# Optimization experiments

Hardware: AMD Instinct MI355X
Metric: run time of the kernel (lower is better)

The kernel has to match this reference:

```python
import jax, jax.numpy as jnp
import numpy as np

N = 50000      # nodes
DEG = 16       # avg degree
E = N * DEG    # edges
F_IN = 256
F_OUT = 128
ALPHA = 0.2    # leaky-relu slope


def setup_inputs() -> dict:
    key = jax.random.key(0)
    k1, k2, k3, k4, k5, k6 = jax.random.split(key, 6)
    x = jax.random.normal(k1, (N, F_IN), dtype=jnp.float32)
    # edges sorted by source (required by the module's `m` construction)
    src = jnp.repeat(jnp.arange(N, dtype=jnp.int32), DEG)
    dst = jax.random.randint(k2, (E,), 0, N, dtype=jnp.int32)
    edge = jnp.stack([src, dst])  # (2, E)
    s_w = 1.414 * np.sqrt(2.0 / (F_IN + F_OUT))   # xavier_normal gain=1.414
    s_a = 1.414 * np.sqrt(2.0 / (1 + 2 * F_OUT))
    W_high = jax.random.normal(k3, (F_IN, F_OUT), jnp.float32) * s_w
    W_low = jax.random.normal(k4, (F_IN, F_OUT), jnp.float32) * s_w
    a_high = jax.random.normal(k5, (1, 2 * F_OUT), jnp.float32) * s_a
    a_low = jax.random.normal(k6, (1, 2 * F_OUT), jnp.float32) * s_a
    return {"x": x, "edge": edge, "W_high": W_high, "W_low": W_low,
            "a_high": a_high, "a_low": a_low}


def _leaky(v):
    return jnp.where(v >= 0, v, ALPHA * v)


def _elu6(v):
    return jnp.minimum(jnp.where(v > 0, v, jnp.expm1(v)), 6.0)


def reference(x, edge, W_high, W_low, a_high, a_low):
    src, dst = edge[0], edge[1]
    n = x.shape[0]
    h_hi = x @ W_high            # (N, F_OUT)
    h_lo = x @ W_low

    # per-edge attention logits: a . [h[src], h[dst]]
    a_hi_s, a_hi_d = a_high[0, :F_OUT], a_high[0, F_OUT:]
    a_lo_s, a_lo_d = a_low[0, :F_OUT], a_low[0, F_OUT:]
    logit_hi = (h_hi @ a_hi_s)[src] + (h_hi @ a_hi_d)[dst]   # (E,)
    logit_lo = (h_lo @ a_lo_s)[src] + (h_lo @ a_lo_d)[dst]
    e_hi = jnp.exp(-_leaky(logit_hi))
    e_lo = jnp.exp(-_leaky(logit_lo))

    # sparse rowsum: spmm(edge, e, [N,N], ones) == segment_sum over src
    rowsum_hi = jax.ops.segment_sum(e_hi, src, num_segments=n)[:, None]
    rowsum_lo = jax.ops.segment_sum(e_lo, src, num_segments=n)[:, None]

    # relu6 (dropout p=0 / eval mode -> identity)
    e_hi = jnp.clip(e_hi, 0.0, 6.0)
    e_lo = jnp.clip(e_lo, 0.0, 6.0)

    # per-edge features, then m @ (.) == segment-sum of edge features by source
    he_hi = h_hi[src] + h_hi[dst]                # (E, F_OUT)
    he_lo = h_lo[src] - h_lo[dst]
    hn_hi = jax.ops.segment_sum(he_hi, src, num_segments=n)  # (N, F_OUT)
    hn_lo = jax.ops.segment_sum(he_lo, src, num_segments=n)

    # spmm(edge, e, [N,N], hn): row i sums e_ij * hn[j] over its edges
    hp_hi = jax.ops.segment_sum(e_hi[:, None] * hn_hi[dst], src, num_segments=n)
    hp_lo = jax.ops.segment_sum(e_lo[:, None] * hn_lo[dst], src, num_segments=n)

    hp_hi = hp_hi / (rowsum_hi + 1e-16)
    hp_lo = hp_lo / (rowsum_lo + 1e-16)
    h_prime = 0.5 * (hp_hi + hp_lo)
    return _elu6(h_prime)  # concat=True branch
```

## Files before the change

kernel.cpp:

```cpp
#include <hip/hip_runtime.h>
#include <hip/hip_bf16.h>
#include <math.h>

#define NN    50000
#define DEG   16
#define FIN   256
#define FOUT  128
#define EE    (NN * DEG)
#define ALPHA 0.2f

#define BM 64
#define BN 256

#define SLW 32

typedef __hip_bfloat16 bf16;
typedef _Float16 f16;
typedef __attribute__((ext_vector_type(8))) _Float16 f16x8;
typedef __attribute__((ext_vector_type(8))) short short8;
typedef __attribute__((ext_vector_type(4))) float f32x4;
typedef __attribute__((ext_vector_type(8))) unsigned short u16x8;
typedef __attribute__((ext_vector_type(8))) unsigned int u32x8;

__global__ __launch_bounds__(256) void split_w_kernel(
    const float* __restrict__ Wh, const float* __restrict__ Wl,
    bf16* __restrict__ Wcat2)
{
    const int k = blockIdx.x;
    const int n = threadIdx.x;
    const float w = (n < FOUT) ? Wh[(size_t)k * FOUT + n]
                               : Wl[(size_t)k * FOUT + (n - FOUT)];
    const bf16 hi = __float2bfloat16(w);
    const bf16 lo = __float2bfloat16(w - __bfloat162float(hi));
    Wcat2[(size_t)n * 512 + k]       = hi;
    Wcat2[(size_t)n * 512 + 256 + k] = lo;
}

__global__ __launch_bounds__(256) void gemm_mfma_kernel(
    const float* __restrict__ x, const bf16* __restrict__ Wcat2,
    const float* __restrict__ a_high, const float* __restrict__ a_low,
    f16* __restrict__ h16, float* __restrict__ sd_s, float* __restrict__ sd_d)
{
    __shared__ bf16 Ah[2][BM * 32];
    __shared__ bf16 Al[2][BM * 32];
    __shared__ bf16 Ba[2][BN * 32];
    __shared__ bf16 Bb[2][BN * 32];

    const int t    = threadIdx.x;
    const int lane = t & 63;
    const int w    = t >> 6;
    const int r0   = blockIdx.x * BM;

    f32x4 acc[4][4] = {};

    const int arow = t >> 2;
    const float* xsrc = x + (size_t)min(r0 + arow, NN - 1) * FIN + (t & 3) * 8;
    const int awaddr = arow * 64 + ((((t & 3)) + (arow >> 1)) & 3) * 16;

    int bro[4], bsl[4];
#pragma unroll
    for (int i = 0; i < 4; ++i) {
        const int idx = t + i * 256;
        bro[i] = idx >> 2;
        bsl[i] = ((idx & 3) - (bro[i] >> 1)) & 3;
    }

    const int lr = lane & 15, lg = lane >> 4;

    float4 xa = *(const float4*)(xsrc + 0);
    float4 xb = *(const float4*)(xsrc + 4);
#pragma unroll
    for (int i = 0; i < 4; ++i) {
        __builtin_amdgcn_global_load_lds(
            (const __attribute__((address_space(1))) void*)
                (Wcat2 + (size_t)bro[i] * 512 + 0 + bsl[i] * 8),
            (__attribute__((address_space(3))) void*)((char*)Ba[0] + (t + i * 256) * 16),
            16, 0, 0);
        __builtin_amdgcn_global_load_lds(
            (const __attribute__((address_space(1))) void*)
                (Wcat2 + (size_t)bro[i] * 512 + 256 + 0 + bsl[i] * 8),
            (__attribute__((address_space(3))) void*)((char*)Bb[0] + (t + i * 256) * 16),
            16, 0, 0);
    }
    {
        short8 hi8, lo8;
        const float f[8] = {xa.x, xa.y, xa.z, xa.w, xb.x, xb.y, xb.z, xb.w};
#pragma unroll
        for (int j = 0; j < 8; ++j) {
            const bf16 h = __float2bfloat16(f[j]);
            const bf16 l = __float2bfloat16(f[j] - __bfloat162float(h));
            ((bf16*)&hi8)[j] = h;
            ((bf16*)&lo8)[j] = l;
        }
        *(short8*)((char*)Ah[0] + awaddr) = hi8;
        *(short8*)((char*)Al[0] + awaddr) = lo8;
    }
    xa = *(const float4*)(xsrc + 32 + 0);
    xb = *(const float4*)(xsrc + 32 + 4);
    __syncthreads();

#pragma unroll
    for (int s = 0; s < 8; ++s) {
        const int cur = s & 1, nxt = cur ^ 1;

        if (s < 7) {
            short8 hi8, lo8;
            const float f[8] = {xa.x, xa.y, xa.z, xa.w, xb.x, xb.y, xb.z, xb.w};
#pragma unroll
            for (int j = 0; j < 8; ++j) {
                const bf16 h = __float2bfloat16(f[j]);
                const bf16 l = __float2bfloat16(f[j] - __bfloat162float(h));
                ((bf16*)&hi8)[j] = h;
                ((bf16*)&lo8)[j] = l;
            }
            *(short8*)((char*)Ah[nxt] + awaddr) = hi8;
            *(short8*)((char*)Al[nxt] + awaddr) = lo8;

            const int c1 = (s + 1) * 32;
#pragma unroll
            for (int i = 0; i < 4; ++i) {
                __builtin_amdgcn_global_load_lds(
                    (const __attribute__((address_space(1))) void*)
                        (Wcat2 + (size_t)bro[i] * 512 + c1 + bsl[i] * 8),
                    (__attribute__((address_space(3))) void*)((char*)Ba[nxt] + (t + i * 256) * 16),
                    16, 0, 0);
                __builtin_amdgcn_global_load_lds(
                    (const __attribute__((address_space(1))) void*)
                        (Wcat2 + (size_t)bro[i] * 512 + 256 + c1 + bsl[i] * 8),
                    (__attribute__((address_space(3))) void*)((char*)Bb[nxt] + (t + i * 256) * 16),
                    16, 0, 0);
            }
            if (s < 6) {
                xa = *(const float4*)(xsrc + (s + 2) * 32 + 0);
                xb = *(const float4*)(xsrc + (s + 2) * 32 + 4);
            }
        }

        short8 fh[4], wa[4], wb[4], fl[4];
#pragma unroll
        for (int mi = 0; mi < 4; ++mi) {
            const int row  = mi * 16 + lr;
            const int slot = (lg + (row >> 1)) & 3;
            fh[mi] = *(const short8*)((const char*)Ah[cur] + row * 64 + slot * 16);
        }
#pragma unroll
        for (int ni = 0; ni < 4; ++ni) {
            const int row  = w * 64 + ni * 16 + lr;
            const int slot = (lg + (row >> 1)) & 3;
            wa[ni] = *(const short8*)((const char*)Ba[cur] + row * 64 + slot * 16);
        }
#pragma unroll
        for (int mi = 0; mi < 4; ++mi)
#pragma unroll
            for (int ni = 0; ni < 4; ++ni)
                acc[mi][ni] = __builtin_amdgcn_mfma_f32_16x16x32_bf16(
                    fh[mi], wa[ni], acc[mi][ni], 0, 0, 0);
#pragma unroll
        for (int ni = 0; ni < 4; ++ni) {
            const int row  = w * 64 + ni * 16 + lr;
            const int slot = (lg + (row >> 1)) & 3;
            wb[ni] = *(const short8*)((const char*)Bb[cur] + row * 64 + slot * 16);
        }
#pragma unroll
        for (int mi = 0; mi < 4; ++mi)
#pragma unroll
            for (int ni = 0; ni < 4; ++ni)
                acc[mi][ni] = __builtin_amdgcn_mfma_f32_16x16x32_bf16(
                    fh[mi], wb[ni], acc[mi][ni], 0, 0, 0);
#pragma unroll
        for (int mi = 0; mi < 4; ++mi) {
            const int row  = mi * 16 + lr;
            const int slot = (lg + (row >> 1)) & 3;
            fl[mi] = *(const short8*)((const char*)Al[cur] + row * 64 + slot * 16);
        }
#pragma unroll
        for (int mi = 0; mi < 4; ++mi)
#pragma unroll
            for (int ni = 0; ni < 4; ++ni)
                acc[mi][ni] = __builtin_amdgcn_mfma_f32_16x16x32_bf16(
                    fl[mi], wa[ni], acc[mi][ni], 0, 0, 0);

        __syncthreads();
    }

    const int slc_base = (w < 2) ? w * 4 : (w - 2) * 4;
    const int off      = ((w < 2) ? 0 : 16) + lr;
#pragma unroll
    for (int mi = 0; mi < 4; ++mi) {
        const int rowb = r0 + mi * 16 + lg * 4;
#pragma unroll
        for (int r = 0; r < 4; ++r) {
            const int row = rowb + r;
            if (row >= NN) continue;
#pragma unroll
            for (int ni = 0; ni < 4; ++ni)
                h16[((size_t)(slc_base + ni) * NN + row) * SLW + off] =
                    (f16)acc[mi][ni][r];
        }
    }

    __syncthreads();

    const float* aa = (w < 2) ? a_high : a_low;
    const int cb = (w < 2) ? w * 64 : (w - 2) * 64;
    float as_[4], ad_[4];
#pragma unroll
    for (int ni = 0; ni < 4; ++ni) {
        as_[ni] = aa[cb + ni * 16 + lr];
        ad_[ni] = aa[FOUT + cb + ni * 16 + lr];
    }
    float* sred = (float*)Ah[0];
#pragma unroll
    for (int mi = 0; mi < 4; ++mi)
#pragma unroll
        for (int r = 0; r < 4; ++r) {
            float ps = 0.f, pd = 0.f;
#pragma unroll
            for (int ni = 0; ni < 4; ++ni) {
                ps += acc[mi][ni][r] * as_[ni];
                pd += acc[mi][ni][r] * ad_[ni];
            }
#pragma unroll
            for (int o = 1; o < 16; o <<= 1) {
                ps += __shfl_xor(ps, o);
                pd += __shfl_xor(pd, o);
            }
            if (lr == 0) {
                const int row = mi * 16 + lg * 4 + r;
                sred[(w * 2 + 0) * 64 + row] = ps;
                sred[(w * 2 + 1) * 64 + row] = pd;
            }
        }
    __syncthreads();
    if (t < 64) {
        const int row = r0 + t;
        if (row < NN) {
            const float s_hi = sred[0 * 64 + t] + sred[2 * 64 + t];
            const float d_hi = sred[1 * 64 + t] + sred[3 * 64 + t];
            const float s_lo = sred[4 * 64 + t] + sred[6 * 64 + t];
            const float d_lo = sred[5 * 64 + t] + sred[7 * 64 + t];
            ((float2*)sd_s)[row] = make_float2(s_hi, s_lo);
            ((float2*)sd_d)[row] = make_float2(d_hi, d_lo);
        }
    }
}

__global__ __launch_bounds__(256) void weight_kernel(
    const int* __restrict__ dst, const float* __restrict__ sd_s,
    const float* __restrict__ sd_d, unsigned short* __restrict__ d16,
    unsigned int* __restrict__ w32)
{
    const int wid  = (blockIdx.x * 256 + threadIdx.x) >> 6;
    const int lane = threadIdx.x & 63;
    if (wid >= NN) return;

    const int e    = lane & 15;
    const int d_my = dst[wid * DEG + e];
    const bool whi = (lane & 16) == 0;
    const float2 s2 = ((const float2*)sd_s)[wid];
    const float2 dd = ((const float2*)sd_d)[d_my];
    const float l   = whi ? (s2.x + dd.x) : (s2.y + dd.y);
    const float ev  = __expf(-(l >= 0.f ? l : ALPHA * l));

    float rs = ev;
    rs += __shfl_xor(rs, 1);
    rs += __shfl_xor(rs, 2);
    rs += __shfl_xor(rs, 4);
    rs += __shfl_xor(rs, 8);
    const float wn = fminf(ev, 6.f) / (rs + 1e-16f);
    const float wl = __shfl(wn, e + 16);

    if (lane < 16) {
        const f16 wh16 = (f16)wn, wl16 = (f16)wl;
        const unsigned a = *(const unsigned short*)&wh16;
        const unsigned b = *(const unsigned short*)&wl16;
        d16[wid * DEG + e] = (unsigned short)d_my;
        w32[wid * DEG + e] = a | (b << 16);
    }
}

__global__ __launch_bounds__(320) void hn_slice_kernel(
    const f16* __restrict__ h16, const unsigned short* __restrict__ d16,
    f16* __restrict__ hn16)
{
    const int sl    = blockIdx.x & 7;
    const int chunk = blockIdx.x >> 3;
    const int wv    = threadIdx.x >> 6;
    const int lane  = threadIdx.x & 63;
    const int k     = lane >> 3;
    const int c     = (lane >> 1) & 3;
    const int hf    = lane & 1;
    const int n     = (chunk * 5 + wv) * 8 + k;

    const char* hsl = (const char*)(h16 + (size_t)sl * NN * SLW);
    const float sgn = (c < 2) ? 1.f : -1.f;
    const unsigned coff = (unsigned)c * 16u;
    const unsigned noff = (unsigned)n * 64u + coff;

    const u16x8 d8 = *(const u16x8*)(d16 + n * DEG + hf * 8);
    const f16x8 own = *(const f16x8*)(hsl + noff);

    float acc[8] = {};
#pragma unroll
    for (int t = 0; t < 8; ++t) {
        const unsigned d = (unsigned)d8[t];
        const f16x8 g = *(const f16x8*)(hsl + (d * 64u + coff));
#pragma unroll
        for (int j = 0; j < 8; ++j) acc[j] = fmaf(sgn, (float)g[j], acc[j]);
    }
#pragma unroll
    for (int j = 0; j < 8; ++j) acc[j] += __shfl_xor(acc[j], 1);

    if (hf == 0) {
        f16x8 o;
#pragma unroll
        for (int j = 0; j < 8; ++j) o[j] = (f16)fmaf((float)own[j], 16.f, acc[j]);
        *(f16x8*)((char*)(hn16 + (size_t)sl * NN * SLW) + noff) = o;
    }
}

__global__ __launch_bounds__(320) void out_slice_kernel(
    const f16* __restrict__ hn16, const unsigned short* __restrict__ d16,
    const unsigned int* __restrict__ w32, float* __restrict__ out)
{
    const int sl    = blockIdx.x & 7;
    const int chunk = blockIdx.x >> 3;
    const int wv    = threadIdx.x >> 6;
    const int lane  = threadIdx.x & 63;
    const int k     = lane >> 3;
    const int c     = (lane >> 1) & 3;
    const int hf    = lane & 1;
    const int n     = (chunk * 5 + wv) * 8 + k;
    const bool chi  = (c < 2);

    const char* hsl = (const char*)(hn16 + (size_t)sl * NN * SLW);
    const unsigned coff = (unsigned)c * 16u;

    const u16x8 d8 = *(const u16x8*)(d16 + n * DEG + hf * 8);
    const u32x8 w8 = *(const u32x8*)(w32 + n * DEG + hf * 8);

    float acc[8] = {};
#pragma unroll
    for (int t = 0; t < 8; ++t) {
        const unsigned wp = w8[t];
        const unsigned short wu = chi ? (unsigned short)(wp & 0xffffu)
                                      : (unsigned short)(wp >> 16);
        const float w = (float)(*(const f16*)&wu);
        const f16x8 g = *(const f16x8*)(hsl + ((unsigned)d8[t] * 64u + coff));
#pragma unroll
        for (int j = 0; j < 8; ++j) acc[j] = fmaf(w, (float)g[j], acc[j]);
    }
#pragma unroll
    for (int j = 0; j < 8; ++j) acc[j] += __shfl_xor(acc[j], 1);

    float4 v0, v1;
#pragma unroll
    for (int j = 0; j < 8; ++j) {
        const float p = __shfl_xor(acc[j], 4);
        float v = 0.5f * (acc[j] + p);
        v = (v > 0.f) ? v : (__expf(v) - 1.f);
        v = fminf(v, 6.f);
        if (j < 4) ((float*)&v0)[j] = v; else ((float*)&v1)[j - 4] = v;
    }
    if (chi && hf == 0) {
        float* op = out + (size_t)n * FOUT + sl * 16 + c * 8;
        *(float4*)op       = v0;
        *(float4*)(op + 4) = v1;
    }
}

extern "C" void kernel_launch(void* const* d_in, const int* in_sizes, int n_in,
                              void* d_out, int out_size, void* d_ws, size_t ws_size,
                              hipStream_t stream)
{
    const float* x      = (const float*)d_in[0];
    const int*   edge   = (const int*)d_in[1];
    const float* Wh     = (const float*)d_in[2];
    const float* Wl     = (const float*)d_in[3];
    const float* a_high = (const float*)d_in[4];
    const float* a_low  = (const float*)d_in[5];
    const int*   dstv   = edge + EE;

    char* ws = (char*)d_ws;
    f16*   h16   = (f16*)ws;
    f16*   hn16  = (f16*)(ws + 25600000);
    bf16*  Wcat2 = (bf16*)(ws + 51200000);
    float* sd_s  = (float*)(ws + 51800000);
    float* sd_d  = (float*)(ws + 52200000);
    unsigned short* d16 = (unsigned short*)(ws + 52600000);
    unsigned int*   w32 = (unsigned int*)(ws + 54400000);

    split_w_kernel<<<dim3(256), dim3(256), 0, stream>>>(Wh, Wl, Wcat2);
    gemm_mfma_kernel<<<dim3((NN + BM - 1) / BM), dim3(256), 0, stream>>>(
        x, Wcat2, a_high, a_low, h16, sd_s, sd_d);
    weight_kernel<<<dim3((NN + 3) / 4), dim3(256), 0, stream>>>(dstv, sd_s, sd_d, d16, w32);
    hn_slice_kernel<<<dim3(8 * 1250), dim3(320), 0, stream>>>(h16, d16, hn16);
    out_slice_kernel<<<dim3(8 * 1250), dim3(320), 0, stream>>>(hn16, d16, w32, (float*)d_out);
}
```

Baseline: 130.3 us.

## Load GEMM weight fragments directly from global memory instead of staging in LDS

The GEMM kernel no longer stages the split hi/lo weight tiles through double-buffered shared memory with async global-to-LDS loads. Each wave now reads its own B fragments straight from global memory, which the weight matrix's small size should keep in L2. All eight x chunks are also loaded and split into bf16 hi/lo parts up front and held in registers. This cuts LDS footprint and the LDS traffic for B, which may raise occupancy, but it raises register pressure and exposes global-load latency on the MFMA path.

```diff
diff --git a/kernel.cpp b/kernel.cpp
--- a/kernel.cpp
+++ b/kernel.cpp
@@ -43,8 +43,6 @@
 {
     __shared__ bf16 Ah[2][BM * 32];
     __shared__ bf16 Al[2][BM * 32];
-    __shared__ bf16 Ba[2][BN * 32];
-    __shared__ bf16 Bb[2][BN * 32];
 
     const int t    = threadIdx.x;
     const int lane = t & 63;
@@ -57,46 +55,27 @@
     const float* xsrc = x + (size_t)min(r0 + arow, NN - 1) * FIN + (t & 3) * 8;
     const int awaddr = arow * 64 + ((((t & 3)) + (arow >> 1)) & 3) * 16;
 
-    int bro[4], bsl[4];
-#pragma unroll
-    for (int i = 0; i < 4; ++i) {
-        const int idx = t + i * 256;
-        bro[i] = idx >> 2;
-        bsl[i] = ((idx & 3) - (bro[i] >> 1)) & 3;
-    }
-
     const int lr = lane & 15, lg = lane >> 4;
 
-    float4 xa = *(const float4*)(xsrc + 0);
-    float4 xb = *(const float4*)(xsrc + 4);
-#pragma unroll
-    for (int i = 0; i < 4; ++i) {
-        __builtin_amdgcn_global_load_lds(
-            (const __attribute__((address_space(1))) void*)
-                (Wcat2 + (size_t)bro[i] * 512 + 0 + bsl[i] * 8),
-            (__attribute__((address_space(3))) void*)((char*)Ba[0] + (t + i * 256) * 16),
-            16, 0, 0);
-        __builtin_amdgcn_global_load_lds(
-            (const __attribute__((address_space(1))) void*)
-                (Wcat2 + (size_t)bro[i] * 512 + 256 + 0 + bsl[i] * 8),
-            (__attribute__((address_space(3))) void*)((char*)Bb[0] + (t + i * 256) * 16),
-            16, 0, 0);
-    }
-    {
-        short8 hi8, lo8;
+    const bf16* bbase = Wcat2 + ((size_t)(w * 64 + lr) * 512) + lg * 8;
+
+    short8 xh[8], xl[8];
+#pragma unroll
+    for (int s = 0; s < 8; ++s) {
+        const float4 xa = *(const float4*)(xsrc + s * 32 + 0);
+        const float4 xb = *(const float4*)(xsrc + s * 32 + 4);
         const float f[8] = {xa.x, xa.y, xa.z, xa.w, xb.x, xb.y, xb.z, xb.w};
 #pragma unroll
         for (int j = 0; j < 8; ++j) {
             const bf16 h = __float2bfloat16(f[j]);
             const bf16 l = __float2bfloat16(f[j] - __bfloat162float(h));
-            ((bf16*)&hi8)[j] = h;
-            ((bf16*)&lo8)[j] = l;
-        }
-        *(short8*)((char*)Ah[0] + awaddr) = hi8;
-        *(short8*)((char*)Al[0] + awaddr) = lo8;
-    }
-    xa = *(const float4*)(xsrc + 32 + 0);
-    xb = *(const float4*)(xsrc + 32 + 4);
+            ((bf16*)&xh[s])[j] = h;
+            ((bf16*)&xl[s])[j] = l;
+        }
+    }
+
+    *(short8*)((char*)Ah[0] + awaddr) = xh[0];
+    *(short8*)((char*)Al[0] + awaddr) = xl[0];
     __syncthreads();
 
 #pragma unroll
@@ -104,39 +83,19 @@
         const int cur = s & 1, nxt = cur ^ 1;
 
         if (s < 7) {
-            short8 hi8, lo8;
-            const float f[8] = {xa.x, xa.y, xa.z, xa.w, xb.x, xb.y, xb.z, xb.w};
-#pragma unroll
-            for (int j = 0; j < 8; ++j) {
-                const bf16 h = __float2bfloat16(f[j]);
-                const bf16 l = __float2bfloat16(f[j] - __bfloat162float(h));
-                ((bf16*)&hi8)[j] = h;
-                ((bf16*)&lo8)[j] = l;
-            }
-            *(short8*)((char*)Ah[nxt] + awaddr) = hi8;
-            *(short8*)((char*)Al[nxt] + awaddr) = lo8;
-
-            const int c1 = (s + 1) * 32;
-#pragma unroll
-            for (int i = 0; i < 4; ++i) {
-                __builtin_amdgcn_global_load_lds(
-                    (const __attribute__((address_space(1))) void*)
-                        (Wcat2 + (size_t)bro[i] * 512 + c1 + bsl[i] * 8),
-                    (__attribute__((address_space(3))) void*)((char*)Ba[nxt] + (t + i * 256) * 16),
-                    16, 0, 0);
-                __builtin_amdgcn_global_load_lds(
-                    (const __attribute__((address_space(1))) void*)
-                        (Wcat2 + (size_t)bro[i] * 512 + 256 + c1 + bsl[i] * 8),
-                    (__attribute__((address_space(3))) void*)((char*)Bb[nxt] + (t + i * 256) * 16),
-                    16, 0, 0);
-            }
-            if (s < 6) {
-                xa = *(const float4*)(xsrc + (s + 2) * 32 + 0);
-                xb = *(const float4*)(xsrc + (s + 2) * 32 + 4);
-            }
-        }
-
-        short8 fh[4], wa[4], wb[4], fl[4];
+            *(short8*)((char*)Ah[nxt] + awaddr) = xh[s + 1];
+            *(short8*)((char*)Al[nxt] + awaddr) = xl[s + 1];
+        }
+
+        short8 wa[4], wb[4];
+#pragma unroll
+        for (int ni = 0; ni < 4; ++ni)
+            wa[ni] = *(const short8*)(bbase + (size_t)ni * 16 * 512 + s * 32);
+#pragma unroll
+        for (int ni = 0; ni < 4; ++ni)
+            wb[ni] = *(const short8*)(bbase + (size_t)ni * 16 * 512 + s * 32 + 256);
+
+        short8 fh[4], fl[4];
 #pragma unroll
         for (int mi = 0; mi < 4; ++mi) {
             const int row  = mi * 16 + lr;
@@ -144,23 +103,11 @@
             fh[mi] = *(const short8*)((const char*)Ah[cur] + row * 64 + slot * 16);
         }
 #pragma unroll
-        for (int ni = 0; ni < 4; ++ni) {
-            const int row  = w * 64 + ni * 16 + lr;
-            const int slot = (lg + (row >> 1)) & 3;
-            wa[ni] = *(const short8*)((const char*)Ba[cur] + row * 64 + slot * 16);
-        }
-#pragma unroll
         for (int mi = 0; mi < 4; ++mi)
 #pragma unroll
             for (int ni = 0; ni < 4; ++ni)
                 acc[mi][ni] = __builtin_amdgcn_mfma_f32_16x16x32_bf16(
                     fh[mi], wa[ni], acc[mi][ni], 0, 0, 0);
-#pragma unroll
-        for (int ni = 0; ni < 4; ++ni) {
-            const int row  = w * 64 + ni * 16 + lr;
-            const int slot = (lg + (row >> 1)) & 3;
-            wb[ni] = *(const short8*)((const char*)Bb[cur] + row * 64 + slot * 16);
-        }
 #pragma unroll
         for (int mi = 0; mi < 4; ++mi)
 #pragma unroll
```

New measurement: 142.5 us. 1.09x slower.
